# Optimization experiments

Measured on AMD Instinct MI355X. Metric: run time of the kernel, lower is better.

The kernel has to match this reference:

```python
import jax, jax.numpy as jnp
import numpy as np

# Hyperparameters mirroring init_kwargs
MAX_ITERS = 100      # ADMM outer iterations
RHO = 1.0            # ADMM penalty
INNER = 20           # PGD steps per x-subproblem
STEP = 5e-05         # fixed PGD step (x_inner_step given, so no svdvals branch)


def setup_inputs() -> dict:
    key = jax.random.key(0)
    kA, kb, kc = jax.random.split(key, 3)
    m, n = 2048, 4096
    A = jax.random.normal(kA, (m, n), dtype=jnp.float32)
    b = jax.random.uniform(kb, (m,), dtype=jnp.float32)
    c = jax.random.uniform(kc, (n,), dtype=jnp.float32)
    return {"A": A, "b": b, "c": c}


def _admm(A, b, c):
    m, n = A.shape

    def outer(carry, _):
        x, s, u = carry
        r = s + b - u  # target for the x-subproblem residual

        # PGD on: min_{x>=0} c^T x + (rho/2)||A x - r||^2
        def pgd(x, _):
            g = c + RHO * (A.T @ (A @ x - r))
            return jnp.maximum(x - STEP * g, 0.0), None

        x, _ = jax.lax.scan(pgd, x, None, length=INNER)

        Ax = A @ x
        s = jnp.maximum(Ax - b + u, 0.0)   # slack update (projection onto >=0)
        u = u + (Ax - s - b)               # scaled dual update
        return (x, s, u), None

    init = (jnp.zeros((n,), A.dtype), jnp.zeros((m,), A.dtype), jnp.zeros((m,), A.dtype))
    (x, s, u), _ = jax.lax.scan(outer, init, None, length=MAX_ITERS)
    lambda_kkt = -RHO * u
    return x, s, u, lambda_kkt


def reference(A, b, c):
    # return_history=False -> torch module returns (x, s, u, lambda_kkt, None);
    # we return the 4 tensor outputs.
    return _admm(A, b, c)
```

## Files before the change

### kernel.cpp

```cpp
#include <hip/hip_runtime.h>
#include <hip/hip_cooperative_groups.h>

namespace cg = cooperative_groups;
typedef unsigned int u32;

#define M_ROWS 2048
#define N_COLS 4096
#define RHO_C 1.0f
#define STEP_C 5e-05f
#define MAX_ITERS_C 100
#define INNER_C 20

__device__ __forceinline__ float aload(const float* p) {
    return __hip_atomic_load(p, __ATOMIC_RELAXED, __HIP_MEMORY_SCOPE_AGENT);
}
__device__ __forceinline__ void astore(float* p, float v) {
    __hip_atomic_store(p, v, __ATOMIC_RELAXED, __HIP_MEMORY_SCOPE_AGENT);
}
__device__ __forceinline__ float2 aload2(const float* p) {
    unsigned long long v = __hip_atomic_load(
        (const unsigned long long*)p, __ATOMIC_RELAXED,
        __HIP_MEMORY_SCOPE_AGENT);
    union { unsigned long long u; float2 f; } c; c.u = v; return c.f;
}
__device__ __forceinline__ u32 aloadu(const u32* p) {
    return __hip_atomic_load(p, __ATOMIC_RELAXED, __HIP_MEMORY_SCOPE_AGENT);
}
__device__ __forceinline__ void astoreu(u32* p, u32 v) {
    __hip_atomic_store(p, v, __ATOMIC_RELAXED, __HIP_MEMORY_SCOPE_AGENT);
}

__device__ __forceinline__ void poll256(const u32* tags, u32 need, int lane) {
    const u32* p = tags + 4 * lane;
    for (;;) {
        u32 t0 = aloadu(p);     u32 t1 = aloadu(p + 1);
        u32 t2 = aloadu(p + 2); u32 t3 = aloadu(p + 3);
        u32 mn = t0 < t1 ? t0 : t1;
        u32 mn2 = t2 < t3 ? t2 : t3;
        mn = mn < mn2 ? mn : mn2;
        if (__ballot(mn < need) == 0ull) return;
        __builtin_amdgcn_s_sleep(1);
    }
}

__global__ __launch_bounds__(1024) void admm_tag(
    const float* __restrict__ A, const float* __restrict__ bvec,
    const float* __restrict__ cvec, float* __restrict__ out,
    float* __restrict__ xbuf,
    float* __restrict__ rtb,
    u32* __restrict__ xtag,
    u32* __restrict__ rtag)
{
    cg::grid_group grid = cg::this_grid();
    const int tid  = threadIdx.x;
    const int blk  = blockIdx.x;
    const int lane = tid & 63;
    const int wave = tid >> 6;
    const int cgp  = wave >> 2;
    const int rq   = wave & 3;

    __shared__ float  abuf[4 * N_COLS];
    __shared__ float4 xs4[1024];
    __shared__ float  red[4][16];
    __shared__ float4 gred[64];
    __shared__ float  wl[16], cw[16];
    __shared__ float  sv[8], uv[8], tpart[16];

    float* xs = reinterpret_cast<float*>(xs4);
    const float4* A4 = reinterpret_cast<const float4*>(A);
    float4* abuf4 = reinterpret_cast<float4*>(abuf);

    if (tid < 16) cw[tid] = cvec[blk * 16 + tid];
    if (tid < 8) { sv[tid] = 0.0f; uv[tid] = 0.0f; }
    if (tid == 0) { astoreu(&xtag[blk], 0u); astoreu(&rtag[blk], 0u); }

    float accM[4][16];
    #pragma unroll
    for (int r = 0; r < 4; ++r)
        #pragma unroll
        for (int k = 0; k < 16; ++k) accM[r][k] = 0.0f;

    for (int i0 = 0; i0 < M_ROWS; i0 += 4) {
        #pragma unroll
        for (int ii = 0; ii < 4; ++ii)
            abuf4[ii * 1024 + tid] = A4[(size_t)(i0 + ii) * 1024 + tid];
        __syncthreads();
        #pragma unroll
        for (int ii = 0; ii < 4; ++ii) {
            const float*  row  = abuf + ii * N_COLS;
            const float4* row4 = abuf4 + ii * 1024;
            float4 av[4];
            #pragma unroll
            for (int q = 0; q < 4; ++q)
                av[q] = row4[256 * cgp + 64 * q + lane];
            float cb[4];
            #pragma unroll
            for (int r = 0; r < 4; ++r) cb[r] = row[blk * 16 + rq * 4 + r];
            #pragma unroll
            for (int r = 0; r < 4; ++r)
                #pragma unroll
                for (int q = 0; q < 4; ++q) {
                    accM[r][4*q+0] = fmaf(cb[r], av[q].x, accM[r][4*q+0]);
                    accM[r][4*q+1] = fmaf(cb[r], av[q].y, accM[r][4*q+1]);
                    accM[r][4*q+2] = fmaf(cb[r], av[q].z, accM[r][4*q+2]);
                    accM[r][4*q+3] = fmaf(cb[r], av[q].w, accM[r][4*q+3]);
                }
        }
        __syncthreads();
    }

    grid.sync();

    for (int outer = 0; outer < MAX_ITERS_C; ++outer) {
        if (outer == 0) {
            abuf[2 * tid]     = bvec[2 * tid];
            abuf[2 * tid + 1] = bvec[2 * tid + 1];
        } else {
            if (wave == 0) poll256(rtag, (u32)outer, lane);
            __syncthreads();
            const float* rb = rtb + (outer & 1) * M_ROWS;
            float2 rv = aload2(rb + 2 * tid);
            abuf[2 * tid]     = rv.x;
            abuf[2 * tid + 1] = rv.y;
        }
        __syncthreads();

        {
            const int p = tid >> 2, gq = tid & 3;
            float4 acc = {0.f, 0.f, 0.f, 0.f};
            #pragma unroll
            for (int k2 = 0; k2 < 8; ++k2) {
                const int i = p + 256 * k2;
                const float tv = abuf[i];
                float4 a = A4[(size_t)i * 1024 + blk * 4 + gq];
                acc.x = fmaf(a.x, tv, acc.x); acc.y = fmaf(a.y, tv, acc.y);
                acc.z = fmaf(a.z, tv, acc.z); acc.w = fmaf(a.w, tv, acc.w);
            }
            #pragma unroll
            for (int off = 4; off < 64; off <<= 1) {
                acc.x += __shfl_xor(acc.x, off);
                acc.y += __shfl_xor(acc.y, off);
                acc.z += __shfl_xor(acc.z, off);
                acc.w += __shfl_xor(acc.w, off);
            }
            if ((lane >> 2) == 0) gred[wave * 4 + gq] = acc;
        }
        __syncthreads();
        if (tid < 4) {
            float4 tot = {0.f, 0.f, 0.f, 0.f};
            #pragma unroll
            for (int w = 0; w < 16; ++w) {
                float4 v = gred[w * 4 + tid];
                tot.x += v.x; tot.y += v.y; tot.z += v.z; tot.w += v.w;
            }
            wl[tid * 4 + 0] = tot.x; wl[tid * 4 + 1] = tot.y;
            wl[tid * 4 + 2] = tot.z; wl[tid * 4 + 3] = tot.w;
        }
        __syncthreads();

        for (int inner = 0; inner < INNER_C; ++inner) {
            const u32 gs = (u32)(outer * INNER_C + inner);

            if (outer == 0 && inner == 0) {
                xs4[tid] = make_float4(0.f, 0.f, 0.f, 0.f);
                __syncthreads();
            } else if (inner > 0) {
                if (wave == 0) poll256(xtag, gs, lane);
                __syncthreads();
                const float* xb = xbuf + (gs & 1) * N_COLS;
                float2 lo = aload2(xb + 4 * tid);
                float2 hi = aload2(xb + 4 * tid + 2);
                xs4[tid] = make_float4(lo.x, lo.y, hi.x, hi.y);
                __syncthreads();
            }

            float4 xq[4];
            #pragma unroll
            for (int q = 0; q < 4; ++q)
                xq[q] = xs4[256 * cgp + 64 * q + lane];

            float4 pd = {0.f, 0.f, 0.f, 0.f};
            #pragma unroll
            for (int q = 0; q < 4; ++q) {
                pd.x = fmaf(accM[0][4*q+0], xq[q].x, pd.x);
                pd.x = fmaf(accM[0][4*q+1], xq[q].y, pd.x);
                pd.x = fmaf(accM[0][4*q+2], xq[q].z, pd.x);
                pd.x = fmaf(accM[0][4*q+3], xq[q].w, pd.x);
                pd.y = fmaf(accM[1][4*q+0], xq[q].x, pd.y);
                pd.y = fmaf(accM[1][4*q+1], xq[q].y, pd.y);
                pd.y = fmaf(accM[1][4*q+2], xq[q].z, pd.y);
                pd.y = fmaf(accM[1][4*q+3], xq[q].w, pd.y);
                pd.z = fmaf(accM[2][4*q+0], xq[q].x, pd.z);
                pd.z = fmaf(accM[2][4*q+1], xq[q].y, pd.z);
                pd.z = fmaf(accM[2][4*q+2], xq[q].z, pd.z);
                pd.z = fmaf(accM[2][4*q+3], xq[q].w, pd.z);
                pd.w = fmaf(accM[3][4*q+0], xq[q].x, pd.w);
                pd.w = fmaf(accM[3][4*q+1], xq[q].y, pd.w);
                pd.w = fmaf(accM[3][4*q+2], xq[q].z, pd.w);
                pd.w = fmaf(accM[3][4*q+3], xq[q].w, pd.w);
            }
            #pragma unroll
            for (int off = 32; off; off >>= 1) {
                pd.x += __shfl_xor(pd.x, off);
                pd.y += __shfl_xor(pd.y, off);
                pd.z += __shfl_xor(pd.z, off);
                pd.w += __shfl_xor(pd.w, off);
            }
            if (lane == 0) {
                red[cgp][rq * 4 + 0] = pd.x;
                red[cgp][rq * 4 + 1] = pd.y;
                red[cgp][rq * 4 + 2] = pd.z;
                red[cgp][rq * 4 + 3] = pd.w;
            }
            __syncthreads();

            if (tid < 16) {
                const float y = red[0][tid] + red[1][tid]
                              + red[2][tid] + red[3][tid];
                const float g = cw[tid] + RHO_C * (y - wl[tid]);
                float xn = xs[blk * 16 + tid] - STEP_C * g;
                xn = xn > 0.f ? xn : 0.f;
                astore(&xbuf[((gs + 1) & 1) * N_COLS + blk * 16 + tid], xn);
            }
            __syncthreads();
            if (tid == 0) astoreu(&xtag[blk], gs + 1);
        }

        {
            const u32 gsf = (u32)((outer + 1) * INNER_C);
            if (wave == 0) poll256(xtag, gsf, lane);
            __syncthreads();
            const float* xb = xbuf + (gsf & 1) * N_COLS;
            float2 lo = aload2(xb + 4 * tid);
            float2 hi = aload2(xb + 4 * tid + 2);
            xs4[tid] = make_float4(lo.x, lo.y, hi.x, hi.y);
            __syncthreads();
        }
        {
            const int r = blk * 8 + (wave >> 1), h = wave & 1;
            const float4* Ar = A4 + (size_t)r * 1024 + h * 512;
            const float4* xh = xs4 + h * 512;
            float4 acc = {0.f, 0.f, 0.f, 0.f};
            #pragma unroll
            for (int it = 0; it < 8; ++it) {
                float4 a = Ar[it * 64 + lane], xv = xh[it * 64 + lane];
                acc.x = fmaf(a.x, xv.x, acc.x); acc.y = fmaf(a.y, xv.y, acc.y);
                acc.z = fmaf(a.z, xv.z, acc.z); acc.w = fmaf(a.w, xv.w, acc.w);
            }
            float d = acc.x + acc.y + acc.z + acc.w;
            #pragma unroll
            for (int off = 32; off; off >>= 1) d += __shfl_xor(d, off);
            if (lane == 0) tpart[wave] = d;
        }
        __syncthreads();
        if (tid < 8) {
            const int i = blk * 8 + tid;
            const float a  = tpart[2 * tid] + tpart[2 * tid + 1];
            const float bb = bvec[i];
            const float uu = uv[tid];
            float sn = a - bb + uu; sn = sn > 0.f ? sn : 0.f;
            const float un = uu + a - sn - bb;
            sv[tid] = sn; uv[tid] = un;
            astore(&rtb[((outer + 1) & 1) * M_ROWS + i], sn + bb - un);
        }
        __syncthreads();
        if (tid == 0) astoreu(&rtag[blk], (u32)(outer + 1));
    }

    if (tid < 16) out[blk * 16 + tid] = xs[blk * 16 + tid];
    if (tid < 8) {
        const int i = blk * 8 + tid;
        out[4096 + i] = sv[tid];
        out[6144 + i] = uv[tid];
        out[8192 + i] = -uv[tid];
    }
}

extern "C" void kernel_launch(void* const* d_in, const int* in_sizes, int n_in,
                              void* d_out, int out_size, void* d_ws, size_t ws_size,
                              hipStream_t stream) {
    const float* A    = (const float*)d_in[0];
    const float* bvec = (const float*)d_in[1];
    const float* cvec = (const float*)d_in[2];
    float* out = (float*)d_out;

    float* ws   = (float*)d_ws;
    float* xbuf = ws;
    float* rtb  = ws + 8192;
    u32*   xtag = (u32*)(ws + 12288);
    u32*   rtag = (u32*)(ws + 12288 + 256);

    void* args[] = { (void*)&A, (void*)&bvec, (void*)&cvec, (void*)&out,
                     (void*)&xbuf, (void*)&rtb, (void*)&xtag, (void*)&rtag };
    hipError_t err = hipLaunchCooperativeKernel((const void*)admm_tag,
                               dim3(256), dim3(1024), args, 0, stream);
    (void)err;
}
```

Before: 11.94 ms.

## Replace per-block tag polling with tagged 64-bit mailbox slots and replicated copies

Each value exchanged between blocks is now packed with its iteration tag in one 64-bit atomic word. Consumers poll their own data slots directly rather than a shared tag array followed by a separate data load, which removes a barrier and a store-then-flag ordering step per exchange. When the workspace is large enough, producers write 8 replicated copies of x and r, and each block reads the copy chosen by its id, to spread polling traffic. The cost is extra producer stores and more workspace. The grid.sync and the tag initialization are also removed, which relies on the workspace never holding stale matching tags from a previous launch.

```diff
diff --git a/kernel.cpp b/kernel.cpp
--- a/kernel.cpp
+++ b/kernel.cpp
@@ -3,6 +3,7 @@
 
 namespace cg = cooperative_groups;
 typedef unsigned int u32;
+typedef unsigned long long u64;
 
 #define M_ROWS 2048
 #define N_COLS 4096
@@ -11,68 +12,63 @@
 #define MAX_ITERS_C 100
 #define INNER_C 20
 
-__device__ __forceinline__ float aload(const float* p) {
+__device__ __forceinline__ u64 ald64(const u64* p) {
     return __hip_atomic_load(p, __ATOMIC_RELAXED, __HIP_MEMORY_SCOPE_AGENT);
 }
-__device__ __forceinline__ void astore(float* p, float v) {
+__device__ __forceinline__ void ast64(u64* p, u64 v) {
     __hip_atomic_store(p, v, __ATOMIC_RELAXED, __HIP_MEMORY_SCOPE_AGENT);
 }
-__device__ __forceinline__ float2 aload2(const float* p) {
-    unsigned long long v = __hip_atomic_load(
-        (const unsigned long long*)p, __ATOMIC_RELAXED,
-        __HIP_MEMORY_SCOPE_AGENT);
-    union { unsigned long long u; float2 f; } c; c.u = v; return c.f;
-}
-__device__ __forceinline__ u32 aloadu(const u32* p) {
-    return __hip_atomic_load(p, __ATOMIC_RELAXED, __HIP_MEMORY_SCOPE_AGENT);
-}
-__device__ __forceinline__ void astoreu(u32* p, u32 v) {
-    __hip_atomic_store(p, v, __ATOMIC_RELAXED, __HIP_MEMORY_SCOPE_AGENT);
-}
-
-__device__ __forceinline__ void poll256(const u32* tags, u32 need, int lane) {
-    const u32* p = tags + 4 * lane;
+__device__ __forceinline__ void push_slot(u64* p, float v, u32 tag) {
+    ast64(p, ((u64)tag << 32) | (u64)__float_as_uint(v));
+}
+__device__ __forceinline__ float4 poll4(const u64* p, u32 tag) {
     for (;;) {
-        u32 t0 = aloadu(p);     u32 t1 = aloadu(p + 1);
-        u32 t2 = aloadu(p + 2); u32 t3 = aloadu(p + 3);
-        u32 mn = t0 < t1 ? t0 : t1;
-        u32 mn2 = t2 < t3 ? t2 : t3;
-        mn = mn < mn2 ? mn : mn2;
-        if (__ballot(mn < need) == 0ull) return;
+        u64 a = ald64(p),     b = ald64(p + 1);
+        u64 c = ald64(p + 2), d = ald64(p + 3);
+        if (((u32)(a >> 32) == tag) & ((u32)(b >> 32) == tag) &
+            ((u32)(c >> 32) == tag) & ((u32)(d >> 32) == tag))
+            return make_float4(__uint_as_float((u32)a), __uint_as_float((u32)b),
+                               __uint_as_float((u32)c), __uint_as_float((u32)d));
         __builtin_amdgcn_s_sleep(1);
     }
 }
-
-__global__ __launch_bounds__(1024) void admm_tag(
+__device__ __forceinline__ float2 poll2(const u64* p, u32 tag) {
+    for (;;) {
+        u64 a = ald64(p), b = ald64(p + 1);
+        if (((u32)(a >> 32) == tag) & ((u32)(b >> 32) == tag))
+            return make_float2(__uint_as_float((u32)a), __uint_as_float((u32)b));
+        __builtin_amdgcn_s_sleep(1);
+    }
+}
+
+__global__ __launch_bounds__(1024) void admm_push(
     const float* __restrict__ A, const float* __restrict__ bvec,
     const float* __restrict__ cvec, float* __restrict__ out,
-    float* __restrict__ xbuf,
-    float* __restrict__ rtb,
-    u32* __restrict__ xtag,
-    u32* __restrict__ rtag)
+    u64* __restrict__ xmb, u64* __restrict__ rmb, int fanout)
 {
-    cg::grid_group grid = cg::this_grid();
     const int tid  = threadIdx.x;
     const int blk  = blockIdx.x;
     const int lane = tid & 63;
     const int wave = tid >> 6;
     const int cgp  = wave >> 2;
     const int rq   = wave & 3;
+    const int cpy  = (fanout == 1) ? 0 : (blk & 7);
 
     __shared__ float  abuf[4 * N_COLS];
     __shared__ float4 xs4[1024];
     __shared__ float  red[4][16];
     __shared__ float4 gred[64];
     __shared__ float  wl[16], cw[16];
-    __shared__ float  sv[8], uv[8], tpart[16];
+    __shared__ float  sv[8], uv[8], tpart[16], rtnew[8];
 
     float* xs = reinterpret_cast<float*>(xs4);
     const float4* A4 = reinterpret_cast<const float4*>(A);
     float4* abuf4 = reinterpret_cast<float4*>(abuf);
+    const u64* xmyc = xmb + (size_t)cpy * 8192;
+    const u64* rmyc = rmb + (size_t)cpy * 4096;
 
     if (tid < 16) cw[tid] = cvec[blk * 16 + tid];
     if (tid < 8) { sv[tid] = 0.0f; uv[tid] = 0.0f; }
-    if (tid == 0) { astoreu(&xtag[blk], 0u); astoreu(&rtag[blk], 0u); }
 
     float accM[4][16];
     #pragma unroll
@@ -109,17 +105,12 @@
         __syncthreads();
     }
 
-    grid.sync();
-
     for (int outer = 0; outer < MAX_ITERS_C; ++outer) {
         if (outer == 0) {
             abuf[2 * tid]     = bvec[2 * tid];
             abuf[2 * tid + 1] = bvec[2 * tid + 1];
         } else {
-            if (wave == 0) poll256(rtag, (u32)outer, lane);
-            __syncthreads();
-            const float* rb = rtb + (outer & 1) * M_ROWS;
-            float2 rv = aload2(rb + 2 * tid);
+            float2 rv = poll2(rmyc + (outer & 1) * 2048 + 2 * tid, (u32)outer);
             abuf[2 * tid]     = rv.x;
             abuf[2 * tid + 1] = rv.y;
         }
@@ -161,16 +152,13 @@
         for (int inner = 0; inner < INNER_C; ++inner) {
             const u32 gs = (u32)(outer * INNER_C + inner);
 
-            if (outer == 0 && inner == 0) {
+            if (gs == 0) {
                 xs4[tid] = make_float4(0.f, 0.f, 0.f, 0.f);
                 __syncthreads();
             } else if (inner > 0) {
-                if (wave == 0) poll256(xtag, gs, lane);
+                float4 xv = poll4(xmyc + (gs & 1) * 4096 + 4 * tid, gs);
                 __syncthreads();
-                const float* xb = xbuf + (gs & 1) * N_COLS;
-                float2 lo = aload2(xb + 4 * tid);
-                float2 hi = aload2(xb + 4 * tid + 2);
-                xs4[tid] = make_float4(lo.x, lo.y, hi.x, hi.y);
+                xs4[tid] = xv;
                 __syncthreads();
             }
 
@@ -214,26 +202,23 @@
             }
             __syncthreads();
 
-            if (tid < 16) {
-                const float y = red[0][tid] + red[1][tid]
-                              + red[2][tid] + red[3][tid];
-                const float g = cw[tid] + RHO_C * (y - wl[tid]);
-                float xn = xs[blk * 16 + tid] - STEP_C * g;
+            if (tid < fanout * 16) {
+                const int dst = tid >> 4, jj = tid & 15;
+                const float y = red[0][jj] + red[1][jj]
+                              + red[2][jj] + red[3][jj];
+                const float g = cw[jj] + RHO_C * (y - wl[jj]);
+                float xn = xs[blk * 16 + jj] - STEP_C * g;
                 xn = xn > 0.f ? xn : 0.f;
-                astore(&xbuf[((gs + 1) & 1) * N_COLS + blk * 16 + tid], xn);
-            }
-            __syncthreads();
-            if (tid == 0) astoreu(&xtag[blk], gs + 1);
+                push_slot(xmb + (size_t)dst * 8192 + ((gs + 1) & 1) * 4096
+                              + blk * 16 + jj, xn, gs + 1);
+            }
         }
 
         {
             const u32 gsf = (u32)((outer + 1) * INNER_C);
-            if (wave == 0) poll256(xtag, gsf, lane);
+            float4 xv = poll4(xmyc + (gsf & 1) * 4096 + 4 * tid, gsf);
             __syncthreads();
-            const float* xb = xbuf + (gsf & 1) * N_COLS;
-            float2 lo = aload2(xb + 4 * tid);
-            float2 hi = aload2(xb + 4 * tid + 2);
-            xs4[tid] = make_float4(lo.x, lo.y, hi.x, hi.y);
+            xs4[tid] = xv;
             __syncthreads();
         }
         {
@@ -261,10 +246,14 @@
             float sn = a - bb + uu; sn = sn > 0.f ? sn : 0.f;
             const float un = uu + a - sn - bb;
             sv[tid] = sn; uv[tid] = un;
-            astore(&rtb[((outer + 1) & 1) * M_ROWS + i], sn + bb - un);
-        }
-        __syncthreads();
-        if (tid == 0) astoreu(&rtag[blk], (u32)(outer + 1));
+            rtnew[tid] = sn + bb - un;
+        }
+        __syncthreads();
+        if (tid < fanout * 8) {
+            const int dst = tid >> 3, jj = tid & 7;
+            push_slot(rmb + (size_t)dst * 4096 + ((outer + 1) & 1) * 2048
+                          + blk * 8 + jj, rtnew[jj], (u32)(outer + 1));
+        }
     }
 
     if (tid < 16) out[blk * 16 + tid] = xs[blk * 16 + tid];
@@ -284,15 +273,13 @@
     const float* cvec = (const float*)d_in[2];
     float* out = (float*)d_out;
 
-    float* ws   = (float*)d_ws;
-    float* xbuf = ws;
-    float* rtb  = ws + 8192;
-    u32*   xtag = (u32*)(ws + 12288);
-    u32*   rtag = (u32*)(ws + 12288 + 256);
+    int fanout = (ws_size >= (size_t)(1 << 20)) ? 8 : 1;
+    u64* xmb = (u64*)d_ws;
+    u64* rmb = xmb + (size_t)fanout * 8192;
 
     void* args[] = { (void*)&A, (void*)&bvec, (void*)&cvec, (void*)&out,
-                     (void*)&xbuf, (void*)&rtb, (void*)&xtag, (void*)&rtag };
-    hipError_t err = hipLaunchCooperativeKernel((const void*)admm_tag,
+                     (void*)&xmb, (void*)&rmb, (void*)&fanout };
+    hipError_t err = hipLaunchCooperativeKernel((const void*)admm_push,
                                dim3(256), dim3(1024), args, 0, stream);
     (void)err;
 }
```

New measurement: 11.43 ms. -4.2%, faster.
